# Kernel tuning notes

Measured on AMD Instinct MI355X. Metric: run time of the kernel, lower is better.

## Reference

```python
import jax, jax.numpy as jnp
import numpy as np

SIZE = 1024      # codebook entries
CODE_DIM = 256   # embedding dim


def setup_inputs() -> dict:
    key = jax.random.key(0)
    k_z, k_w = jax.random.split(key)
    z = jax.random.normal(k_z, (8, CODE_DIM, 16, 32, 32), dtype=jnp.float32)
    # init.uniform_(weight, -1/size, 1/size)
    codebook = jax.random.uniform(
        k_w, (SIZE, CODE_DIM), dtype=jnp.float32,
        minval=-1.0 / SIZE, maxval=1.0 / SIZE)
    return {"z": z, "codebook": codebook}


def reference(z, codebook):
    bs, d, t, h, w = z.shape
    # tokens: [N, d] with N = bs*t*h*w (matches permute(0,2,3,4,1).reshape(-1,d))
    zf = jnp.transpose(z, (0, 2, 3, 4, 1)).reshape(-1, d)
    # squared-distance expansion instead of materializing [size, N, d]:
    # ||z - e||^2 = ||z||^2 - 2 z.e + ||e||^2 ; argmin identical to argmin of norm
    d2 = (jnp.sum(zf * zf, axis=1, keepdims=True)
          - 2.0 * (zf @ codebook.T)
          + jnp.sum(codebook * codebook, axis=1))  # [N, size]
    encoding_indices = jnp.argmin(d2, axis=-1).reshape(bs, t, h, w)
    # gather + permute back to [bs, d, t, h, w]
    quantized = jnp.transpose(codebook[encoding_indices], (0, 4, 1, 2, 3))
    st = z + jax.lax.stop_gradient(quantized - z)  # straight-through output
    return (quantized, st, encoding_indices)
```

## Files before the change

### kernel.cpp

```cpp
#include <hip/hip_runtime.h>
#include <stdint.h>


constexpr int Dd  = 256;
constexpr int SPB = 16384;
constexpr int Nn  = 131072;
constexpr int Kk  = 1024;
constexpr int CCAP = 16;
#define WWIN 2.2e-3f

typedef short short8 __attribute__((ext_vector_type(8)));
typedef float v4f    __attribute__((ext_vector_type(4)));

__device__ __forceinline__ unsigned bf16pk(float a, float b){
  unsigned ua = __float_as_uint(a), ub = __float_as_uint(b);
  ua = (ua + 0x7fffu + ((ua >> 16) & 1u)) >> 16;
  ub = (ub + 0x7fffu + ((ub >> 16) & 1u)) & 0xffff0000u;
  return ua | ub;
}
__device__ __forceinline__ short8 frg(uint4 u){
  union { uint4 a; short8 b; } x; x.a = u; return x.b;
}
__device__ __forceinline__ v4f mfma16(short8 a, short8 b, v4f c){
  return __builtin_amdgcn_mfma_f32_16x16x32_bf16(a, b, c, 0, 0, 0);
}
__device__ __forceinline__ void dma16(const void* g, void* l){
  __builtin_amdgcn_global_load_lds((const __attribute__((address_space(1))) void*)g,
                                   (__attribute__((address_space(3))) void*)l, 16, 0, 0);
}

__global__ __launch_bounds__(64) void cnorm_k(const float* __restrict__ cb,
                                              float* __restrict__ cn){
  const int k = blockIdx.x, l = threadIdx.x;
  const float* row = cb + (size_t)k * Dd;
  float s = 0.f;
  #pragma unroll
  for (int c = 0; c < Dd; c += 64){ float v = row[c + l]; s += v * v; }
  #pragma unroll
  for (int off = 32; off > 0; off >>= 1) s += __shfl_down(s, off, 64);
  if (l == 0) cn[k] = s;
}

__global__ __launch_bounds__(256) void cconv_k(const float* __restrict__ cb,
                                               uint4* __restrict__ Bg){
  const int cc = blockIdx.x, n = threadIdx.x;
  const float* row = cb + (size_t)(cc * 256 + n) * Dd;
  for (int dc = 0; dc < 8; dc++){
    float v[32];
    const float4* rp = (const float4*)(row + dc * 32);
    #pragma unroll
    for (int q = 0; q < 8; q++){
      float4 f = rp[q]; v[4*q]=f.x; v[4*q+1]=f.y; v[4*q+2]=f.z; v[4*q+3]=f.w;
    }
    unsigned hv[16];
    #pragma unroll
    for (int p = 0; p < 16; p++) hv[p] = bf16pk(v[2*p], v[2*p+1]);
    size_t base = ((size_t)cc * 8 + dc) * 1024;
    #pragma unroll
    for (int kq = 0; kq < 4; kq++)
      Bg[base + (size_t)kq*256 + n] = make_uint4(hv[4*kq],hv[4*kq+1],hv[4*kq+2],hv[4*kq+3]);
  }
}

__global__ __launch_bounds__(512, 4) void vq_sweep_k(const float* __restrict__ z,
                                                     const uint4* __restrict__ Bg,
                                                     const float* __restrict__ cnG,
                                                     int* __restrict__ cntW,
                                                     unsigned short* __restrict__ candW,
                                                     int* __restrict__ abestW){
  __shared__ uint4 Bs[2][2048];
  __shared__ float cnS[1024];

  const int tid = threadIdx.x, bId = blockIdx.x;
  const int w = tid >> 6, ln = tid & 63;
  const int li = ln & 15, lq = ln >> 4;

  const int tok0 = bId * 256;
  const int b = tok0 >> 14;
  const int s0 = tok0 & 16383;
  const float* zb = z + (size_t)b * Dd * SPB + s0;
  short8 aF[2][8];
  #pragma unroll
  for (int mi = 0; mi < 2; mi++){
    const int tl = w*32 + mi*16 + li;
    #pragma unroll
    for (int kk = 0; kk < 8; kk++){
      float v[8];
      #pragma unroll
      for (int j = 0; j < 8; j++)
        v[j] = zb[(size_t)(kk*32 + lq*8 + j) * SPB + tl];
      union { unsigned u[4]; short8 s8; } x;
      #pragma unroll
      for (int p = 0; p < 4; p++) x.u[p] = bf16pk(v[2*p], v[2*p+1]);
      aF[mi][kk] = x.s8;
    }
  }

  if (w < 4) dma16((const uint4*)cnG + w*64 + ln, (uint4*)&cnS[w*256]);
  int bOff[4];
  #pragma unroll
  for (int j = 0; j < 4; j++){
    const int f = j*512 + tid;
    bOff[j] = (f >> 8)*1024 + ((f >> 6) & 3)*256 + (f & 63);
  }
  #pragma unroll
  for (int j = 0; j < 4; j++)
    dma16(Bg + bOff[j], &Bs[0][j*512 + w*64]);

  unsigned bestR[8]; int cntR[8];
  #pragma unroll
  for (int i = 0; i < 8; i++){ bestR[i] = 0xFFFFFFFFu; cntR[i] = 0; }

  for (int c = 0; c < 16; c++){
    if (c < 15){
      const int cn1 = c + 1;
      const size_t srcB = (size_t)(cn1 >> 2)*8192 + (size_t)((cn1 & 3)*64);
      uint4* dstB = &Bs[cn1 & 1][0];
      #pragma unroll
      for (int j = 0; j < 4; j++)
        dma16(Bg + srcB + bOff[j], dstB + j*512 + w*64);
      asm volatile("s_waitcnt vmcnt(4)" ::: "memory");
    } else {
      asm volatile("s_waitcnt vmcnt(0)" ::: "memory");
    }
    __builtin_amdgcn_s_barrier();
    asm volatile("" ::: "memory");

    v4f acc[2][4];
    const v4f vz = {0.f, 0.f, 0.f, 0.f};
    #pragma unroll
    for (int mi = 0; mi < 2; mi++)
      #pragma unroll
      for (int ni = 0; ni < 4; ni++) acc[mi][ni] = vz;

    const uint4* Bbase = &Bs[c & 1][lq*64 + li];
    __builtin_amdgcn_s_setprio(1);
    #pragma unroll
    for (int kk = 0; kk < 8; kk++){
      short8 b0 = frg(Bbase[kk*256 +  0]);
      short8 b1 = frg(Bbase[kk*256 + 16]);
      short8 b2 = frg(Bbase[kk*256 + 32]);
      short8 b3 = frg(Bbase[kk*256 + 48]);
      #pragma unroll
      for (int mi = 0; mi < 2; mi++){
        acc[mi][0] = mfma16(aF[mi][kk], b0, acc[mi][0]);
        acc[mi][1] = mfma16(aF[mi][kk], b1, acc[mi][1]);
        acc[mi][2] = mfma16(aF[mi][kk], b2, acc[mi][2]);
        acc[mi][3] = mfma16(aF[mi][kk], b3, acc[mi][3]);
      }
    }
    __builtin_amdgcn_s_setprio(0);

    float cnv[4];
    #pragma unroll
    for (int ni = 0; ni < 4; ni++) cnv[ni] = cnS[c*64 + ni*16 + li];

    const int codeB = c*64 + li;
    #pragma unroll
    for (int mi = 0; mi < 2; mi++){
      #pragma unroll
      for (int r = 0; r < 4; r++){
        const int i = mi*4 + r;
        unsigned pm = 0xFFFFFFFFu;
        #pragma unroll
        for (int ni = 0; ni < 4; ni++){
          float s = fmaf(acc[mi][ni][r], -2.0f, cnv[ni]);
          unsigned u = __float_as_uint(s);
          u ^= (unsigned)((int)u >> 31) | 0x80000000u;
          unsigned p = (u & 0xFFFFFC00u) | (unsigned)(codeB + ni*16);
          acc[mi][ni][r] = __uint_as_float(p);
          pm = (pm < p) ? pm : p;
        }
        unsigned pmw = pm;
        #pragma unroll
        for (int off = 1; off < 16; off <<= 1){
          unsigned o = (unsigned)__shfl_xor((int)pmw, off, 16);
          pmw = (pmw < o) ? pmw : o;
        }
        bestR[i] = (bestR[i] < pmw) ? bestR[i] : pmw;
        unsigned bp = bestR[i] & 0xFFFFFC00u;
        unsigned fb = (bp & 0x80000000u) ? (bp ^ 0x80000000u) : ~bp;
        float thrf = __uint_as_float(fb) + WWIN;
        unsigned tu = __float_as_uint(thrf);
        tu ^= (unsigned)((int)tu >> 31) | 0x80000000u;
        tu |= 1023u;
        if (__any(pm <= tu)){
          const int tok = tok0 + w*32 + mi*16 + lq*4 + r;
          int base = cntR[i];
          #pragma unroll
          for (int ni = 0; ni < 4; ni++){
            const unsigned p = __float_as_uint(acc[mi][ni][r]);
            const bool pass = (p <= tu);
            unsigned long long bal = __ballot(pass);
            const unsigned bq = (unsigned)(bal >> (lq*16)) & 0xFFFFu;
            if (pass){
              int pos = base + __popc(bq & ((1u << li) - 1u));
              if (pos < CCAP)
                candW[(size_t)tok*CCAP + pos] = (unsigned short)(p & 1023u);
            }
            base += __popc(bq);
          }
          cntR[i] = base;
        }
      }
    }
    __builtin_amdgcn_s_barrier();
    asm volatile("" ::: "memory");
  }

  if (li == 0){
    #pragma unroll
    for (int mi = 0; mi < 2; mi++)
      #pragma unroll
      for (int r = 0; r < 4; r++){
        const int i = mi*4 + r;
        const int tok = tok0 + w*32 + mi*16 + lq*4 + r;
        cntW[tok] = cntR[i];
        abestW[tok] = (int)(bestR[i] & 1023u);
      }
  }
}

__global__ __launch_bounds__(256) void vq_rescore_k(const float* __restrict__ z,
                                                    const float* __restrict__ cb,
                                                    const float* __restrict__ cnG,
                                                    const int* __restrict__ cntW,
                                                    const unsigned short* __restrict__ candW,
                                                    const int* __restrict__ abestW,
                                                    int* __restrict__ idsW,
                                                    float* __restrict__ out){
  const int tok = blockIdx.x * 256 + threadIdx.x;
  const int b = tok >> 14, s = tok & 16383;
  const float* zr = z + (size_t)b * Dd * SPB + s;

  int n = cntW[tok];
  const bool ovf = (n > CCAP);
  if (ovf) n = CCAP;
  unsigned short cds[CCAP];
  *(uint4*)&cds[0] = *(const uint4*)&candW[(size_t)tok * CCAP];
  *(uint4*)&cds[8] = *(const uint4*)&candW[(size_t)tok * CCAP + 8];

  float bv = 3.4e38f; int bi = 0x7fffffff;
  float znl = 0.f;
  const int ngroups = (n + 3) >> 2;
  const int total = ovf ? ngroups + 1 : ngroups;

  for (int g = 0; g < total; g++){
    int idxs[4];
    #pragma unroll
    for (int ss = 0; ss < 4; ss++){
      int slot = g*4 + ss; if (slot >= n) slot = n - 1;
      idxs[ss] = (g < ngroups) ? (int)cds[slot] : abestW[tok];
    }
    const float* cr0 = cb + (size_t)idxs[0] * Dd;
    const float* cr1 = cb + (size_t)idxs[1] * Dd;
    const float* cr2 = cb + (size_t)idxs[2] * Dd;
    const float* cr3 = cb + (size_t)idxs[3] * Dd;
    float a0=0.f, a1=0.f, a2=0.f, a3=0.f, za=0.f;
    for (int d = 0; d < Dd; d += 8){
      float zv[8];
      #pragma unroll
      for (int j = 0; j < 8; j++) zv[j] = zr[(size_t)(d + j) * SPB];
      float4 c0a = *(const float4*)(cr0 + d), c0b = *(const float4*)(cr0 + d + 4);
      float4 c1a = *(const float4*)(cr1 + d), c1b = *(const float4*)(cr1 + d + 4);
      float4 c2a = *(const float4*)(cr2 + d), c2b = *(const float4*)(cr2 + d + 4);
      float4 c3a = *(const float4*)(cr3 + d), c3b = *(const float4*)(cr3 + d + 4);
      float cv0[8] = {c0a.x,c0a.y,c0a.z,c0a.w,c0b.x,c0b.y,c0b.z,c0b.w};
      float cv1[8] = {c1a.x,c1a.y,c1a.z,c1a.w,c1b.x,c1b.y,c1b.z,c1b.w};
      float cv2[8] = {c2a.x,c2a.y,c2a.z,c2a.w,c2b.x,c2b.y,c2b.z,c2b.w};
      float cv3[8] = {c3a.x,c3a.y,c3a.z,c3a.w,c3b.x,c3b.y,c3b.z,c3b.w};
      #pragma unroll
      for (int j = 0; j < 8; j++){
        if (g == 0) za = fmaf(zv[j], zv[j], za);
        a0 = fmaf(zv[j], cv0[j], a0);
        a1 = fmaf(zv[j], cv1[j], a1);
        a2 = fmaf(zv[j], cv2[j], a2);
        a3 = fmaf(zv[j], cv3[j], a3);
      }
    }
    if (g == 0) znl = za;
    float av[4] = {a0, a1, a2, a3};
    const int lim = (g < ngroups) ? n : 1;
    #pragma unroll
    for (int ss = 0; ss < 4; ss++){
      if (g*4 + ss < lim || (g >= ngroups && ss == 0)){
        float t  = znl - 2.0f * av[ss];
        float d2 = t + cnG[idxs[ss]];
        if (d2 < bv || (d2 == bv && idxs[ss] < bi)){ bv = d2; bi = idxs[ss]; }
      }
    }
  }
  idsW[tok] = bi;
  out[(size_t)2 * Nn * Dd + tok] = (float)bi;
}

__global__ __launch_bounds__(256) void vq_gather_k(const float* __restrict__ cb,
                                                   const int* __restrict__ idsW,
                                                   float* __restrict__ out){
  __shared__ float tile[64][129];
  __shared__ int lid[64];
  const int tid = threadIdx.x, blk = blockIdx.x;
  const int b = blk >> 8, s0 = (blk & 255) * 64;
  if (tid < 64) lid[tid] = idsW[b * SPB + s0 + tid];
  __syncthreads();

  const int r2 = tid >> 7, c = tid & 127;
  const int s = tid & 63, cq = tid >> 6;
  float* qb  = out + (size_t)b * Dd * SPB + s0 + s;
  float* stb = qb + (size_t)Nn * Dd;

  for (int ch = 0; ch < 2; ch++){
    #pragma unroll 4
    for (int t0 = 0; t0 < 64; t0 += 2){
      const int row = t0 + r2;
      tile[row][c] = cb[(size_t)lid[row] * Dd + ch*128 + c];
    }
    __syncthreads();
    #pragma unroll 8
    for (int i = 0; i < 32; i++){
      const int cc2 = i*4 + cq;
      const float v = tile[s][cc2];
      const size_t off = (size_t)(ch*128 + cc2) * SPB;
      qb[off]  = v;
      stb[off] = v;
    }
    __syncthreads();
  }
}

#define MICRO_STEP(WITH_ZN)                                                    \
    {                                                                          \
        float4 a0 = *(const float4*)&As[d][ty * 8];                            \
        float4 a1 = *(const float4*)&As[d][ty * 8 + 4];                        \
        float4 b0 = *(const float4*)&Bs[d][tx * 8];                            \
        float4 b1 = *(const float4*)&Bs[d][tx * 8 + 4];                        \
        float a[8] = {a0.x, a0.y, a0.z, a0.w, a1.x, a1.y, a1.z, a1.w};         \
        float bb[8] = {b0.x, b0.y, b0.z, b0.w, b1.x, b1.y, b1.z, b1.w};        \
        _Pragma("unroll")                                                      \
        for (int i = 0; i < 8; i++) {                                          \
            _Pragma("unroll")                                                  \
            for (int j = 0; j < 8; j++) acc[i][j] += a[i] * bb[j];             \
            if (WITH_ZN) zn[i] += a[i] * a[i];                                 \
        }                                                                      \
    }

__global__ __launch_bounds__(256) void vq_k(const float* __restrict__ z,
                                            const float* __restrict__ cb,
                                            const float* __restrict__ cn,
                                            float* __restrict__ out){
  __shared__ float As[16][128];
  __shared__ float Bs[16][132];
  __shared__ int   idsf[128];
  const int tid = threadIdx.x;
  const int tx = tid & 15, ty = tid >> 4;
  const int blk = blockIdx.x;
  const int b = blk >> 7, sb = (blk & 127) * 128;
  const float* zb = z + (size_t)b * Dd * SPB + sb;
  float bestv[8]; int besti[8]; float zn[8];
  #pragma unroll
  for (int i = 0; i < 8; i++){ bestv[i] = 3.4e38f; besti[i] = 0; zn[i] = 0.f; }
  const int am = tid & 127, ad = tid >> 7;
  const int bd = tid & 15,  bk = tid >> 4;
  for (int cc = 0; cc < 8; cc++){
    float acc[8][8];
    #pragma unroll
    for (int i = 0; i < 8; i++)
      #pragma unroll
      for (int j = 0; j < 8; j++) acc[i][j] = 0.f;
    for (int dc = 0; dc < 16; dc++){
      #pragma unroll
      for (int r = 0; r < 8; r++){
        const int d = ad + r * 2;
        As[d][am] = zb[(size_t)(dc*16 + d) * SPB + am];
      }
      #pragma unroll
      for (int r = 0; r < 8; r++){
        const int k = bk + r * 16;
        Bs[bd][k] = cb[(size_t)(cc*128 + k) * Dd + dc*16 + bd];
      }
      __syncthreads();
      if (cc == 0){
        #pragma unroll
        for (int d = 0; d < 16; d++) MICRO_STEP(1)
      } else {
        #pragma unroll
        for (int d = 0; d < 16; d++) MICRO_STEP(0)
      }
      __syncthreads();
    }
    const float* cnp = cn + cc*128 + tx*8;
    float4 c0 = *(const float4*)cnp;
    float4 c1 = *(const float4*)(cnp + 4);
    float cv[8] = {c0.x, c0.y, c0.z, c0.w, c1.x, c1.y, c1.z, c1.w};
    #pragma unroll
    for (int i = 0; i < 8; i++){
      #pragma unroll
      for (int j = 0; j < 8; j++){
        float t  = zn[i] - 2.0f * acc[i][j];
        float d2 = t + cv[j];
        int   ix = cc*128 + tx*8 + j;
        if (d2 < bestv[i]){ bestv[i] = d2; besti[i] = ix; }
      }
    }
  }
  #pragma unroll
  for (int i = 0; i < 8; i++){
    float v = bestv[i]; int ix = besti[i];
    #pragma unroll
    for (int off = 8; off > 0; off >>= 1){
      float ov = __shfl_down(v, off, 16);
      int   oi = __shfl_down(ix, off, 16);
      if (ov < v || (ov == v && oi < ix)){ v = ov; ix = oi; }
    }
    if (tx == 0) idsf[ty*8 + i] = ix;
  }
  __syncthreads();
  if (tid < 128) out[(size_t)2*Nn*Dd + (size_t)blk*128 + tid] = (float)idsf[tid];
  const int m = tid & 127, cg = tid >> 7;
  const int myidx = idsf[m];
  const float* crow = cb + (size_t)myidx * Dd + cg*128;
  float* q  = out + (size_t)b * Dd * SPB + (size_t)cg * 128 * SPB + sb + m;
  float* st = q + (size_t)Nn * Dd;
  #pragma unroll 8
  for (int r = 0; r < 128; r++){
    const float v = crow[r];
    q[(size_t)r * SPB]  = v;
    st[(size_t)r * SPB] = v;
  }
}

extern "C" void kernel_launch(void* const* d_in, const int* in_sizes, int n_in,
                              void* d_out, int out_size, void* d_ws, size_t ws_size,
                              hipStream_t stream){
  const float* z  = (const float*)d_in[0];
  const float* cb = (const float*)d_in[1];
  float* out = (float*)d_out;

  const size_t BG_B  = (size_t)4 * 8 * 1024 * 16;
  const size_t CN_B  = (size_t)Kk * 4;
  const size_t CNT_B = (size_t)Nn * 4;
  const size_t CAN_B = (size_t)Nn * CCAP * 2;
  const size_t ABW_B = (size_t)Nn * 4;
  const size_t IDS_B = (size_t)Nn * 4;
  const size_t NEED = BG_B + CN_B + CNT_B + CAN_B + ABW_B + IDS_B;

  if (ws_size >= NEED){
    uint8_t* ws = (uint8_t*)d_ws;
    size_t o = 0;
    uint4* Bg   = (uint4*)(ws + o);          o += BG_B;
    float* cnG  = (float*)(ws + o);          o += CN_B;
    int*   cntW = (int*)(ws + o);            o += CNT_B;
    unsigned short* candW = (unsigned short*)(ws + o); o += CAN_B;
    int*   abW  = (int*)(ws + o);            o += ABW_B;
    int*   idsW = (int*)(ws + o);            o += IDS_B;

    cnorm_k<<<Kk, 64, 0, stream>>>(cb, cnG);
    cconv_k<<<4, 256, 0, stream>>>(cb, Bg);
    vq_sweep_k<<<Nn/256, 512, 0, stream>>>(z, Bg, cnG, cntW, candW, abW);
    vq_rescore_k<<<Nn/256, 256, 0, stream>>>(z, cb, cnG, cntW, candW, abW, idsW, out);
    vq_gather_k<<<Nn/64, 256, 0, stream>>>(cb, idsW, out);
  } else {
    float* cn = (float*)d_ws;
    cnorm_k<<<Kk, 64, 0, stream>>>(cb, cn);
    vq_k<<<Nn/128, 256, 0, stream>>>(z, cb, cn, out);
  }
}
```

Before: 717.7 us.

## Resolve single-candidate tokens in sweep and rescore only a compacted heavy list

The sweep kernel now writes the final index directly for tokens whose candidate window holds exactly one code, and appends the remaining tokens to a global heavy list through a block-local compaction and one atomic per block. The rescore kernel then walks only that list in a grid-stride loop instead of rescoring every token in fp32. The sweep also halves the tokens per block (one 16-row tile per wave instead of two) to raise the block count and lower register use, and it recomputes the threshold only when the running best improves. The trade-offs are less B-fragment reuse per LDS load, extra atomics, and a rescore workload whose size depends on the data.

After: 687.2 us. 4.3% less time.

```diff
diff --git a/kernel.cpp b/kernel.cpp
--- a/kernel.cpp
+++ b/kernel.cpp
@@ -30,8 +30,10 @@
 }
 
 __global__ __launch_bounds__(64) void cnorm_k(const float* __restrict__ cb,
-                                              float* __restrict__ cn){
+                                              float* __restrict__ cn,
+                                              int* __restrict__ heavyCnt){
   const int k = blockIdx.x, l = threadIdx.x;
+  if (k == 0 && l == 0) heavyCnt[0] = 0;
   const float* row = cb + (size_t)k * Dd;
   float s = 0.f;
   #pragma unroll
@@ -67,54 +69,60 @@
                                                      const float* __restrict__ cnG,
                                                      int* __restrict__ cntW,
                                                      unsigned short* __restrict__ candW,
-                                                     int* __restrict__ abestW){
+                                                     int* __restrict__ abestW,
+                                                     int* __restrict__ heavyCnt,
+                                                     int* __restrict__ heavyList,
+                                                     int* __restrict__ idsW,
+                                                     float* __restrict__ out){
   __shared__ uint4 Bs[2][2048];
   __shared__ float cnS[1024];
+  __shared__ int hN;
+  __shared__ int gBase;
+  __shared__ int hT[128];
 
   const int tid = threadIdx.x, bId = blockIdx.x;
   const int w = tid >> 6, ln = tid & 63;
   const int li = ln & 15, lq = ln >> 4;
 
-  const int tok0 = bId * 256;
+  if (tid == 0) hN = 0;
+
+  if (w < 4) dma16((const uint4*)cnG + w*64 + ln, (uint4*)&cnS[w*256]);
+  int bOff[4];
+  #pragma unroll
+  for (int j = 0; j < 4; j++){
+    const int f = j*512 + tid;
+    bOff[j] = (f >> 8)*1024 + ((f >> 6) & 3)*256 + (f & 63);
+  }
+  #pragma unroll
+  for (int j = 0; j < 4; j++)
+    dma16(Bg + bOff[j], &Bs[0][j*512 + w*64]);
+
+  const int tok0 = bId * 128;
   const int b = tok0 >> 14;
   const int s0 = tok0 & 16383;
   const float* zb = z + (size_t)b * Dd * SPB + s0;
-  short8 aF[2][8];
-  #pragma unroll
-  for (int mi = 0; mi < 2; mi++){
-    const int tl = w*32 + mi*16 + li;
-    #pragma unroll
-    for (int kk = 0; kk < 8; kk++){
-      float v[8];
-      #pragma unroll
-      for (int j = 0; j < 8; j++)
-        v[j] = zb[(size_t)(kk*32 + lq*8 + j) * SPB + tl];
-      union { unsigned u[4]; short8 s8; } x;
-      #pragma unroll
-      for (int p = 0; p < 4; p++) x.u[p] = bf16pk(v[2*p], v[2*p+1]);
-      aF[mi][kk] = x.s8;
-    }
-  }
-
-  if (w < 4) dma16((const uint4*)cnG + w*64 + ln, (uint4*)&cnS[w*256]);
-  int bOff[4];
-  #pragma unroll
-  for (int j = 0; j < 4; j++){
-    const int f = j*512 + tid;
-    bOff[j] = (f >> 8)*1024 + ((f >> 6) & 3)*256 + (f & 63);
-  }
-  #pragma unroll
-  for (int j = 0; j < 4; j++)
-    dma16(Bg + bOff[j], &Bs[0][j*512 + w*64]);
-
-  unsigned bestR[8]; int cntR[8];
-  #pragma unroll
-  for (int i = 0; i < 8; i++){ bestR[i] = 0xFFFFFFFFu; cntR[i] = 0; }
+  short8 aF[8];
+  const int tl = w*16 + li;
+  #pragma unroll
+  for (int kk = 0; kk < 8; kk++){
+    float v[8];
+    #pragma unroll
+    for (int j = 0; j < 8; j++)
+      v[j] = zb[(size_t)(kk*32 + lq*8 + j) * SPB + tl];
+    union { unsigned u[4]; short8 s8; } x;
+    #pragma unroll
+    for (int p = 0; p < 4; p++) x.u[p] = bf16pk(v[2*p], v[2*p+1]);
+    aF[kk] = x.s8;
+  }
+
+  unsigned bestR[4], thrU[4]; int cntR[4];
+  #pragma unroll
+  for (int i = 0; i < 4; i++){ bestR[i] = 0xFFFFFFFFu; thrU[i] = 0u; cntR[i] = 0; }
 
   for (int c = 0; c < 16; c++){
     if (c < 15){
       const int cn1 = c + 1;
-      const size_t srcB = (size_t)(cn1 >> 2)*8192 + (size_t)((cn1 & 3)*64);
+      const int srcB = (cn1 >> 2)*8192 + (cn1 & 3)*64;
       uint4* dstB = &Bs[cn1 & 1][0];
       #pragma unroll
       for (int j = 0; j < 4; j++)
@@ -126,12 +134,10 @@
     __builtin_amdgcn_s_barrier();
     asm volatile("" ::: "memory");
 
-    v4f acc[2][4];
+    v4f acc[4];
     const v4f vz = {0.f, 0.f, 0.f, 0.f};
     #pragma unroll
-    for (int mi = 0; mi < 2; mi++)
-      #pragma unroll
-      for (int ni = 0; ni < 4; ni++) acc[mi][ni] = vz;
+    for (int ni = 0; ni < 4; ni++) acc[ni] = vz;
 
     const uint4* Bbase = &Bs[c & 1][lq*64 + li];
     __builtin_amdgcn_s_setprio(1);
@@ -141,13 +147,10 @@
       short8 b1 = frg(Bbase[kk*256 + 16]);
       short8 b2 = frg(Bbase[kk*256 + 32]);
       short8 b3 = frg(Bbase[kk*256 + 48]);
-      #pragma unroll
-      for (int mi = 0; mi < 2; mi++){
-        acc[mi][0] = mfma16(aF[mi][kk], b0, acc[mi][0]);
-        acc[mi][1] = mfma16(aF[mi][kk], b1, acc[mi][1]);
-        acc[mi][2] = mfma16(aF[mi][kk], b2, acc[mi][2]);
-        acc[mi][3] = mfma16(aF[mi][kk], b3, acc[mi][3]);
-      }
+      acc[0] = mfma16(aF[kk], b0, acc[0]);
+      acc[1] = mfma16(aF[kk], b1, acc[1]);
+      acc[2] = mfma16(aF[kk], b2, acc[2]);
+      acc[3] = mfma16(aF[kk], b3, acc[3]);
     }
     __builtin_amdgcn_s_setprio(0);
 
@@ -157,51 +160,50 @@
 
     const int codeB = c*64 + li;
     #pragma unroll
-    for (int mi = 0; mi < 2; mi++){
-      #pragma unroll
-      for (int r = 0; r < 4; r++){
-        const int i = mi*4 + r;
-        unsigned pm = 0xFFFFFFFFu;
-        #pragma unroll
-        for (int ni = 0; ni < 4; ni++){
-          float s = fmaf(acc[mi][ni][r], -2.0f, cnv[ni]);
-          unsigned u = __float_as_uint(s);
-          u ^= (unsigned)((int)u >> 31) | 0x80000000u;
-          unsigned p = (u & 0xFFFFFC00u) | (unsigned)(codeB + ni*16);
-          acc[mi][ni][r] = __uint_as_float(p);
-          pm = (pm < p) ? pm : p;
-        }
-        unsigned pmw = pm;
-        #pragma unroll
-        for (int off = 1; off < 16; off <<= 1){
-          unsigned o = (unsigned)__shfl_xor((int)pmw, off, 16);
-          pmw = (pmw < o) ? pmw : o;
-        }
-        bestR[i] = (bestR[i] < pmw) ? bestR[i] : pmw;
-        unsigned bp = bestR[i] & 0xFFFFFC00u;
+    for (int r = 0; r < 4; r++){
+      unsigned pv[4];
+      unsigned pm = 0xFFFFFFFFu;
+      #pragma unroll
+      for (int ni = 0; ni < 4; ni++){
+        float s = fmaf(acc[ni][r], -2.0f, cnv[ni]);
+        unsigned u = __float_as_uint(s);
+        u ^= (unsigned)((int)u >> 31) | 0x80000000u;
+        unsigned p = (u & 0xFFFFFC00u) | (unsigned)(codeB + ni*16);
+        pv[ni] = p;
+        pm = (pm < p) ? pm : p;
+      }
+      unsigned pmw = pm;
+      #pragma unroll
+      for (int off = 1; off < 16; off <<= 1){
+        unsigned o = (unsigned)__shfl_xor((int)pmw, off, 16);
+        pmw = (pmw < o) ? pmw : o;
+      }
+      if (pmw <= bestR[r]){
+        bestR[r] = pmw;
+        unsigned bp = pmw & 0xFFFFFC00u;
         unsigned fb = (bp & 0x80000000u) ? (bp ^ 0x80000000u) : ~bp;
         float thrf = __uint_as_float(fb) + WWIN;
         unsigned tu = __float_as_uint(thrf);
         tu ^= (unsigned)((int)tu >> 31) | 0x80000000u;
-        tu |= 1023u;
-        if (__any(pm <= tu)){
-          const int tok = tok0 + w*32 + mi*16 + lq*4 + r;
-          int base = cntR[i];
-          #pragma unroll
-          for (int ni = 0; ni < 4; ni++){
-            const unsigned p = __float_as_uint(acc[mi][ni][r]);
-            const bool pass = (p <= tu);
-            unsigned long long bal = __ballot(pass);
-            const unsigned bq = (unsigned)(bal >> (lq*16)) & 0xFFFFu;
-            if (pass){
-              int pos = base + __popc(bq & ((1u << li) - 1u));
-              if (pos < CCAP)
-                candW[(size_t)tok*CCAP + pos] = (unsigned short)(p & 1023u);
-            }
-            base += __popc(bq);
+        thrU[r] = tu | 1023u;
+      }
+      if (__any(pm <= thrU[r])){
+        const int tok = tok0 + w*16 + lq*4 + r;
+        int base = cntR[r];
+        #pragma unroll
+        for (int ni = 0; ni < 4; ni++){
+          const unsigned p = pv[ni];
+          const bool pass = (p <= thrU[r]);
+          unsigned long long bal = __ballot(pass);
+          const unsigned bq = (unsigned)(bal >> (lq*16)) & 0xFFFFu;
+          if (pass){
+            int pos = base + __popc(bq & ((1u << li) - 1u));
+            if (pos < CCAP)
+              candW[(size_t)tok*CCAP + pos] = (unsigned short)(p & 1023u);
           }
-          cntR[i] = base;
+          base += __popc(bq);
         }
+        cntR[r] = base;
       }
     }
     __builtin_amdgcn_s_barrier();
@@ -210,15 +212,24 @@
 
   if (li == 0){
     #pragma unroll
-    for (int mi = 0; mi < 2; mi++)
-      #pragma unroll
-      for (int r = 0; r < 4; r++){
-        const int i = mi*4 + r;
-        const int tok = tok0 + w*32 + mi*16 + lq*4 + r;
-        cntW[tok] = cntR[i];
-        abestW[tok] = (int)(bestR[i] & 1023u);
-      }
-  }
+    for (int r = 0; r < 4; r++){
+      const int tok = tok0 + w*16 + lq*4 + r;
+      if (cntR[r] == 1){
+        const int code = (int)(bestR[r] & 1023u);
+        idsW[tok] = code;
+        out[(size_t)2 * Nn * Dd + tok] = (float)code;
+      } else {
+        int p = atomicAdd(&hN, 1);
+        hT[p] = tok;
+        cntW[tok] = cntR[r];
+        abestW[tok] = (int)(bestR[r] & 1023u);
+      }
+    }
+  }
+  __syncthreads();
+  if (tid == 0) gBase = hN ? atomicAdd(heavyCnt, hN) : 0;
+  __syncthreads();
+  if (tid < hN) heavyList[gBase + tid] = hT[tid];
 }
 
 __global__ __launch_bounds__(256) void vq_rescore_k(const float* __restrict__ z,
@@ -227,71 +238,76 @@
                                                     const int* __restrict__ cntW,
                                                     const unsigned short* __restrict__ candW,
                                                     const int* __restrict__ abestW,
+                                                    const int* __restrict__ heavyCnt,
+                                                    const int* __restrict__ heavyList,
                                                     int* __restrict__ idsW,
                                                     float* __restrict__ out){
-  const int tok = blockIdx.x * 256 + threadIdx.x;
-  const int b = tok >> 14, s = tok & 16383;
-  const float* zr = z + (size_t)b * Dd * SPB + s;
-
-  int n = cntW[tok];
-  const bool ovf = (n > CCAP);
-  if (ovf) n = CCAP;
-  unsigned short cds[CCAP];
-  *(uint4*)&cds[0] = *(const uint4*)&candW[(size_t)tok * CCAP];
-  *(uint4*)&cds[8] = *(const uint4*)&candW[(size_t)tok * CCAP + 8];
-
-  float bv = 3.4e38f; int bi = 0x7fffffff;
-  float znl = 0.f;
-  const int ngroups = (n + 3) >> 2;
-  const int total = ovf ? ngroups + 1 : ngroups;
-
-  for (int g = 0; g < total; g++){
-    int idxs[4];
-    #pragma unroll
-    for (int ss = 0; ss < 4; ss++){
-      int slot = g*4 + ss; if (slot >= n) slot = n - 1;
-      idxs[ss] = (g < ngroups) ? (int)cds[slot] : abestW[tok];
-    }
-    const float* cr0 = cb + (size_t)idxs[0] * Dd;
-    const float* cr1 = cb + (size_t)idxs[1] * Dd;
-    const float* cr2 = cb + (size_t)idxs[2] * Dd;
-    const float* cr3 = cb + (size_t)idxs[3] * Dd;
-    float a0=0.f, a1=0.f, a2=0.f, a3=0.f, za=0.f;
-    for (int d = 0; d < Dd; d += 8){
-      float zv[8];
-      #pragma unroll
-      for (int j = 0; j < 8; j++) zv[j] = zr[(size_t)(d + j) * SPB];
-      float4 c0a = *(const float4*)(cr0 + d), c0b = *(const float4*)(cr0 + d + 4);
-      float4 c1a = *(const float4*)(cr1 + d), c1b = *(const float4*)(cr1 + d + 4);
-      float4 c2a = *(const float4*)(cr2 + d), c2b = *(const float4*)(cr2 + d + 4);
-      float4 c3a = *(const float4*)(cr3 + d), c3b = *(const float4*)(cr3 + d + 4);
-      float cv0[8] = {c0a.x,c0a.y,c0a.z,c0a.w,c0b.x,c0b.y,c0b.z,c0b.w};
-      float cv1[8] = {c1a.x,c1a.y,c1a.z,c1a.w,c1b.x,c1b.y,c1b.z,c1b.w};
-      float cv2[8] = {c2a.x,c2a.y,c2a.z,c2a.w,c2b.x,c2b.y,c2b.z,c2b.w};
-      float cv3[8] = {c3a.x,c3a.y,c3a.z,c3a.w,c3b.x,c3b.y,c3b.z,c3b.w};
-      #pragma unroll
-      for (int j = 0; j < 8; j++){
-        if (g == 0) za = fmaf(zv[j], zv[j], za);
-        a0 = fmaf(zv[j], cv0[j], a0);
-        a1 = fmaf(zv[j], cv1[j], a1);
-        a2 = fmaf(zv[j], cv2[j], a2);
-        a3 = fmaf(zv[j], cv3[j], a3);
-      }
-    }
-    if (g == 0) znl = za;
-    float av[4] = {a0, a1, a2, a3};
-    const int lim = (g < ngroups) ? n : 1;
-    #pragma unroll
-    for (int ss = 0; ss < 4; ss++){
-      if (g*4 + ss < lim || (g >= ngroups && ss == 0)){
-        float t  = znl - 2.0f * av[ss];
-        float d2 = t + cnG[idxs[ss]];
-        if (d2 < bv || (d2 == bv && idxs[ss] < bi)){ bv = d2; bi = idxs[ss]; }
-      }
-    }
-  }
-  idsW[tok] = bi;
-  out[(size_t)2 * Nn * Dd + tok] = (float)bi;
+  const int hc = heavyCnt[0];
+  for (int i = blockIdx.x * 256 + threadIdx.x; i < hc; i += gridDim.x * 256){
+    const int tok = heavyList[i];
+    const int b = tok >> 14, s = tok & 16383;
+    const float* zr = z + (size_t)b * Dd * SPB + s;
+
+    int n = cntW[tok];
+    const bool ovf = (n > CCAP);
+    if (ovf) n = CCAP;
+    unsigned short cds[CCAP];
+    *(uint4*)&cds[0] = *(const uint4*)&candW[(size_t)tok * CCAP];
+    *(uint4*)&cds[8] = *(const uint4*)&candW[(size_t)tok * CCAP + 8];
+
+    float bv = 3.4e38f; int bi = 0x7fffffff;
+    float znl = 0.f;
+    const int ngroups = (n + 3) >> 2;
+    const int total = ovf ? ngroups + 1 : ngroups;
+
+    for (int g = 0; g < total; g++){
+      int idxs[4];
+      #pragma unroll
+      for (int ss = 0; ss < 4; ss++){
+        int slot = g*4 + ss; if (slot >= n) slot = n - 1;
+        idxs[ss] = (g < ngroups) ? (int)cds[slot] : abestW[tok];
+      }
+      const float* cr0 = cb + (size_t)idxs[0] * Dd;
+      const float* cr1 = cb + (size_t)idxs[1] * Dd;
+      const float* cr2 = cb + (size_t)idxs[2] * Dd;
+      const float* cr3 = cb + (size_t)idxs[3] * Dd;
+      float a0=0.f, a1=0.f, a2=0.f, a3=0.f, za=0.f;
+      for (int d = 0; d < Dd; d += 8){
+        float zv[8];
+        #pragma unroll
+        for (int j = 0; j < 8; j++) zv[j] = zr[(size_t)(d + j) * SPB];
+        float4 c0a = *(const float4*)(cr0 + d), c0b = *(const float4*)(cr0 + d + 4);
+        float4 c1a = *(const float4*)(cr1 + d), c1b = *(const float4*)(cr1 + d + 4);
+        float4 c2a = *(const float4*)(cr2 + d), c2b = *(const float4*)(cr2 + d + 4);
+        float4 c3a = *(const float4*)(cr3 + d), c3b = *(const float4*)(cr3 + d + 4);
+        float cv0[8] = {c0a.x,c0a.y,c0a.z,c0a.w,c0b.x,c0b.y,c0b.z,c0b.w};
+        float cv1[8] = {c1a.x,c1a.y,c1a.z,c1a.w,c1b.x,c1b.y,c1b.z,c1b.w};
+        float cv2[8] = {c2a.x,c2a.y,c2a.z,c2a.w,c2b.x,c2b.y,c2b.z,c2b.w};
+        float cv3[8] = {c3a.x,c3a.y,c3a.z,c3a.w,c3b.x,c3b.y,c3b.z,c3b.w};
+        #pragma unroll
+        for (int j = 0; j < 8; j++){
+          if (g == 0) za = fmaf(zv[j], zv[j], za);
+          a0 = fmaf(zv[j], cv0[j], a0);
+          a1 = fmaf(zv[j], cv1[j], a1);
+          a2 = fmaf(zv[j], cv2[j], a2);
+          a3 = fmaf(zv[j], cv3[j], a3);
+        }
+      }
+      if (g == 0) znl = za;
+      float av[4] = {a0, a1, a2, a3};
+      const int lim = (g < ngroups) ? n : 1;
+      #pragma unroll
+      for (int ss = 0; ss < 4; ss++){
+        if (g*4 + ss < lim || (g >= ngroups && ss == 0)){
+          float t  = znl - 2.0f * av[ss];
+          float d2 = t + cnG[idxs[ss]];
+          if (d2 < bv || (d2 == bv && idxs[ss] < bi)){ bv = d2; bi = idxs[ss]; }
+        }
+      }
+    }
+    idsW[tok] = bi;
+    out[(size_t)2 * Nn * Dd + tok] = (float)bi;
+  }
 }
 
 __global__ __launch_bounds__(256) void vq_gather_k(const float* __restrict__ cb,
@@ -442,7 +458,9 @@
   const size_t CAN_B = (size_t)Nn * CCAP * 2;
   const size_t ABW_B = (size_t)Nn * 4;
   const size_t IDS_B = (size_t)Nn * 4;
-  const size_t NEED = BG_B + CN_B + CNT_B + CAN_B + ABW_B + IDS_B;
+  const size_t HC_B  = 256;
+  const size_t HL_B  = (size_t)Nn * 4;
+  const size_t NEED = BG_B + CN_B + CNT_B + CAN_B + ABW_B + IDS_B + HC_B + HL_B;
 
   if (ws_size >= NEED){
     uint8_t* ws = (uint8_t*)d_ws;
@@ -453,15 +471,19 @@
     unsigned short* candW = (unsigned short*)(ws + o); o += CAN_B;
     int*   abW  = (int*)(ws + o);            o += ABW_B;
     int*   idsW = (int*)(ws + o);            o += IDS_B;
-
-    cnorm_k<<<Kk, 64, 0, stream>>>(cb, cnG);
+    int*   hCnt = (int*)(ws + o);            o += HC_B;
+    int*   hLst = (int*)(ws + o);            o += HL_B;
+
+    cnorm_k<<<Kk, 64, 0, stream>>>(cb, cnG, hCnt);
     cconv_k<<<4, 256, 0, stream>>>(cb, Bg);
-    vq_sweep_k<<<Nn/256, 512, 0, stream>>>(z, Bg, cnG, cntW, candW, abW);
-    vq_rescore_k<<<Nn/256, 256, 0, stream>>>(z, cb, cnG, cntW, candW, abW, idsW, out);
+    vq_sweep_k<<<Nn/128, 512, 0, stream>>>(z, Bg, cnG, cntW, candW, abW,
+                                           hCnt, hLst, idsW, out);
+    vq_rescore_k<<<Nn/256, 256, 0, stream>>>(z, cb, cnG, cntW, candW, abW,
+                                             hCnt, hLst, idsW, out);
     vq_gather_k<<<Nn/64, 256, 0, stream>>>(cb, idsW, out);
   } else {
     float* cn = (float*)d_ws;
-    cnorm_k<<<Kk, 64, 0, stream>>>(cb, cn);
+    cnorm_k<<<Kk, 64, 0, stream>>>(cb, cn, (int*)(cn + Kk));
     vq_k<<<Nn/128, 256, 0, stream>>>(z, cb, cn, out);
   }
 }
```
